# Optimization experiments

Measured on AMD Instinct MI355X. Metric: run time of the kernel, lower is better.

Reference implementation:

```python
import jax, jax.numpy as jnp
import numpy as np

N = 50000      # nodes
E = 800000     # edges per relation graph
D = 128        # embedding_size
L = 3          # gcn_layers
R = 4          # relations (n, poi, s, d)
ATT_SLOPE = 0.2   # GATConv negative_slope
ACT_SLOPE = 0.01  # F.leaky_relu default
BN_EPS = 1e-5


def setup_inputs() -> dict:
    key = jax.random.key(0)
    ks = jax.random.split(key, 8)
    features = jax.random.normal(ks[0], (N, D), jnp.float32)
    rel_emb = jax.random.normal(ks[1], (R, D), jnp.float32)
    edge_index = jax.random.randint(ks[2], (R, 2, E), 0, N, dtype=jnp.int64)
    s = 1.0 / np.sqrt(D)
    gat_W = jax.random.normal(ks[3], (L, D, D), jnp.float32) * s
    gat_asrc = jax.random.normal(ks[4], (L, D), jnp.float32) * s
    gat_adst = jax.random.normal(ks[5], (L, D), jnp.float32) * s
    gat_b = jnp.zeros((L, D), jnp.float32)
    bn_gamma = jnp.ones((L - 1, D), jnp.float32)
    bn_beta = jnp.zeros((L - 1, D), jnp.float32)
    rel_W = jax.random.normal(ks[6], (L, D, D), jnp.float32) * s
    rel_b = jax.random.normal(ks[7], (L, D), jnp.float32) * s
    return dict(features=features, rel_emb=rel_emb, edge_index=edge_index,
                gat_W=gat_W, gat_asrc=gat_asrc, gat_adst=gat_adst, gat_b=gat_b,
                bn_gamma=bn_gamma, bn_beta=bn_beta, rel_W=rel_W, rel_b=rel_b)


def gat_conv(x, edges, W, a_src, a_dst, b):
    # PyG GATConv, heads=1, no attention dropout (eval path).
    h = x @ W                                   # [N, D]
    src, dst = edges[0], edges[1]               # messages src -> dst
    e = jax.nn.leaky_relu(h[src] @ a_src + h[dst] @ a_dst, ATT_SLOPE)  # [E]
    e_max = jax.ops.segment_max(e, dst, num_segments=N)
    e_max = jnp.where(jnp.isfinite(e_max), e_max, 0.0)
    p = jnp.exp(e - e_max[dst])                 # unnormalized attn [E]
    denom = jax.ops.segment_sum(p, dst, num_segments=N)
    msg = jax.ops.segment_sum(p[:, None] * h[src], dst, num_segments=N)
    return msg / (denom[:, None] + 1e-16) + b


def batch_norm(x, gamma, beta):
    mu = x.mean(0)
    var = x.var(0)  # biased, as BN uses for normalization
    return gamma * (x - mu) * jax.lax.rsqrt(var + BN_EPS) + beta


def reference(features, rel_emb, edge_index, gat_W, gat_asrc, gat_adst, gat_b,
              bn_gamma, bn_beta, rel_W, rel_b):
    embs = [features, features, features, features]
    rels = [rel_emb[k] for k in range(R)]
    edges = [edge_index[k] for k in range(R)]
    for i in range(L - 1):
        for k in range(R):
            out = gat_conv(embs[k] * rels[k], edges[k],
                           gat_W[i], gat_asrc[i], gat_adst[i], gat_b[i])
            bn = batch_norm(out, bn_gamma[i], bn_beta[i])
            embs[k] = embs[k] + jax.nn.leaky_relu(bn, ACT_SLOPE)
            rels[k] = rels[k] @ rel_W[i].T + rel_b[i]
    for k in range(R):
        embs[k] = gat_conv(embs[k] * rels[k], edges[k],
                           gat_W[-1], gat_asrc[-1], gat_adst[-1], gat_b[-1])
        rels[k] = rels[k] @ rel_W[-1].T + rel_b[-1]
    return (embs[0], embs[1], embs[2], embs[3], rels[0], rels[1], rels[2], rels[3])
```

## Files before the change

kernel.cpp:

```cpp
#include <hip/hip_runtime.h>

#define NN 50000
#define NE 800000
#define D  128
#define RT 32
#define NB 196
#define ND ((size_t)NN * D)
#define RNG 6250

typedef unsigned short u16;
typedef unsigned int   u32;
typedef long long      ll64;

__device__ __forceinline__ float bf2f(u16 v) {
  return __uint_as_float(((u32)v) << 16);
}
__device__ __forceinline__ u16 f2bf(float f) {
  u32 u = __float_as_uint(f);
  u32 r = u + 0x7fffu + ((u >> 16) & 1u);
  return (u16)(r >> 16);
}
__device__ __forceinline__ float bflo(u32 u) { return __uint_as_float(u << 16); }
__device__ __forceinline__ float bfhi(u32 u) { return __uint_as_float(u & 0xffff0000u); }
__device__ __forceinline__ float ldf(const void* p, size_t i, int isf32) {
  return isf32 ? ((const float*)p)[i] : bf2f(((const u16*)p)[i]);
}
__device__ __forceinline__ int lde(const void* p, size_t i, int isi64) {
  return isi64 ? (int)((const ll64*)p)[i] : ((const int*)p)[i];
}

__global__ void k_detect(const void* __restrict__ feat, const void* __restrict__ edges,
                         int* __restrict__ flags) {
  __shared__ int cnt0, cnt1;
  int t = threadIdx.x;
  if (t == 0) { cnt0 = 0; cnt1 = 0; }
  __syncthreads();
  float v = ((const float*)feat)[t];
  float av = fabsf(v);
  if (av == 0.f || (av >= 1e-8f && av <= 1e4f)) atomicAdd(&cnt0, 1);
  if (t < 128) {
    if (((const int*)edges)[2 * t + 1] != 0) atomicAdd(&cnt1, 1);
  }
  __syncthreads();
  if (t == 0) {
    flags[0] = (cnt0 >= 240) ? 1 : 0;
    flags[1] = (cnt1 == 0) ? 1 : 0;
  }
}

__global__ void k_sent(float* __restrict__ out, int n) {
  int i = blockIdx.x * 256 + threadIdx.x;
  if (i < n) out[i] = 3000.0f;
}

__global__ void k_init(const void* __restrict__ feat, float* __restrict__ out,
                       const int* __restrict__ flags) {
  int isf32 = flags[0];
  int k = blockIdx.y;
  size_t i = (size_t)blockIdx.x * 256 + threadIdx.x;
  float4 v;
  if (isf32) {
    v = ((const float4*)feat)[i];
  } else {
    uint2 u = ((const uint2*)feat)[i];
    v = make_float4(bflo(u.x), bfhi(u.x), bflo(u.y), bfhi(u.y));
  }
  ((float4*)out)[(size_t)k * (ND / 4) + i] = v;
}

__global__ void k_count(const void* __restrict__ edges, int* __restrict__ deg,
                        const int* __restrict__ flags) {
  int isi64 = flags[1];
  int bid = blockIdx.x;
  int r8 = bid & 7;
  int k = (bid >> 3) & 3;
  int e = (bid >> 5) * 256 + threadIdx.x;
  int dst = lde(edges, (size_t)k * 2 * NE + NE + e, isi64);
  if (dst / RNG == r8) atomicAdd(&deg[k * NN + dst], 1);
}

__global__ void k_bsum(const int* __restrict__ deg, int* __restrict__ bsum) {
  int k = blockIdx.y, b = blockIdx.x, t = threadIdx.x;
  __shared__ int sh[256];
  int idx = b * 256 + t;
  sh[t] = (idx < NN) ? deg[k * NN + idx] : 0;
  __syncthreads();
  for (int off = 128; off; off >>= 1) {
    if (t < off) sh[t] += sh[t + off];
    __syncthreads();
  }
  if (t == 0) bsum[k * NB + b] = sh[0];
}

__global__ void k_bscan(const int* __restrict__ bsum, int* __restrict__ boff) {
  __shared__ int sh[256];
  int t = threadIdx.x;
  for (int k = 0; k < 4; k++) {
    int v = (t < NB) ? bsum[k * NB + t] : 0;
    sh[t] = v;
    __syncthreads();
    for (int off = 1; off < 256; off <<= 1) {
      int a = (t >= off) ? sh[t - off] : 0;
      __syncthreads();
      sh[t] += a;
      __syncthreads();
    }
    if (t < NB) boff[k * NB + t] = sh[t] - v;
    __syncthreads();
  }
}

__global__ void k_place(const int* __restrict__ deg, const int* __restrict__ boff,
                        int* __restrict__ rowp, int* __restrict__ cur) {
  int k = blockIdx.y, b = blockIdx.x, t = threadIdx.x;
  __shared__ int sh[256];
  int idx = b * 256 + t;
  int v = (idx < NN) ? deg[k * NN + idx] : 0;
  sh[t] = v;
  __syncthreads();
  for (int off = 1; off < 256; off <<= 1) {
    int a = (t >= off) ? sh[t - off] : 0;
    __syncthreads();
    sh[t] += a;
    __syncthreads();
  }
  int incl = boff[k * NB + b] + sh[t];
  if (idx < NN) {
    rowp[(size_t)k * (NN + 1) + idx + 1] = incl;
    cur[k * NN + idx] = incl - v;
  }
  if (b == 0 && t == 0) rowp[(size_t)k * (NN + 1)] = 0;
}

__global__ void k_scatter(const void* __restrict__ edges, int* __restrict__ cur,
                          u16* __restrict__ colx, const int* __restrict__ flags) {
  int isi64 = flags[1];
  int bid = blockIdx.x;
  int r8 = bid & 7;
  int k = (bid >> 3) & 3;
  int e = (bid >> 5) * 256 + threadIdx.x;
  int src = lde(edges, (size_t)k * 2 * NE + e, isi64);
  int dst = lde(edges, (size_t)k * 2 * NE + NE + e, isi64);
  if (dst / RNG == r8) {
    int pos = atomicAdd(&cur[k * NN + dst], 1);
    colx[(size_t)k * NE + pos] = (u16)src;
  }
}

__global__ void k_prep(const void* __restrict__ gatW, const void* __restrict__ asrc,
                       const void* __restrict__ adst, const void* __restrict__ rel_emb,
                       const float* __restrict__ relc, int layer,
                       float* __restrict__ Bm, float* __restrict__ asf, float* __restrict__ adf,
                       float* __restrict__ colsum, float* __restrict__ colsq,
                       const int* __restrict__ flags) {
  int isf32 = flags[0];
  int k = blockIdx.x;
  int r = threadIdx.x;
  float rv = (layer == 0) ? ldf(rel_emb, (size_t)k * D + r, isf32) : relc[k * D + r];
  size_t Wo = (size_t)layer * D * D + (size_t)r * D;
  float* Bk = Bm + (size_t)k * D * D;
  for (int c = 0; c < D; c++)
    Bk[r * D + c] = rv * ldf(gatW, Wo + c, isf32);
  asf[k * D + r] = ldf(asrc, (size_t)layer * D + r, isf32);
  adf[k * D + r] = ldf(adst, (size_t)layer * D + r, isf32);
  #pragma unroll
  for (int i = 0; i < 8; i++) {
    colsum[((size_t)k * 8 + i) * D + r] = 0.f;
    colsq[((size_t)k * 8 + i) * D + r] = 0.f;
  }
}

__launch_bounds__(256)
__global__ void k_gemm(const float* __restrict__ xbase, const float* __restrict__ Bm,
                       const float* __restrict__ asf, const float* __restrict__ adf,
                       u32* __restrict__ hb, float* __restrict__ av_s, float* __restrict__ av_d) {
  int k = blockIdx.y;
  const float* x = xbase + (size_t)k * ND;
  const float* Bk = Bm + (size_t)k * D * D;
  u32* hbk = hb + (size_t)k * NN * 64;

  __shared__ float xl[RT * D];
  int t = threadIdx.x;
  int row0 = blockIdx.x * RT;

  for (int i = t; i < RT * D / 4; i += 256) {
    int r = i >> 5;
    int row = row0 + r;
    float4 v = make_float4(0.f, 0.f, 0.f, 0.f);
    if (row < NN) v = ((const float4*)(x + (size_t)row * D))[i & 31];
    ((float4*)xl)[i] = v;
  }
  __syncthreads();

  int cg = t & 31, rg = t >> 5;
  float acc0[4], acc1[4], acc2[4], acc3[4];
  #pragma unroll
  for (int j = 0; j < 4; j++) { acc0[j] = 0; acc1[j] = 0; acc2[j] = 0; acc3[j] = 0; }
  const float* Bp = Bk + cg * 4;
  const float* xp = xl + (rg * 4) * D;
  for (int kk = 0; kk < D; kk += 4) {
    float4 b0 = *(const float4*)(Bp + (kk    ) * D);
    float4 b1 = *(const float4*)(Bp + (kk + 1) * D);
    float4 b2 = *(const float4*)(Bp + (kk + 2) * D);
    float4 b3 = *(const float4*)(Bp + (kk + 3) * D);
    #pragma unroll
    for (int j = 0; j < 4; j++) {
      float4 x4 = *(const float4*)(xp + j * D + kk);
      acc0[j] += x4.x * b0.x + x4.y * b1.x + x4.z * b2.x + x4.w * b3.x;
      acc1[j] += x4.x * b0.y + x4.y * b1.y + x4.z * b2.y + x4.w * b3.y;
      acc2[j] += x4.x * b0.z + x4.y * b1.z + x4.z * b2.z + x4.w * b3.z;
      acc3[j] += x4.x * b0.w + x4.y * b1.w + x4.z * b2.w + x4.w * b3.w;
    }
  }
  #pragma unroll
  for (int j = 0; j < 4; j++) {
    int row = row0 + rg * 4 + j;
    if (row < NN) {
      uint2 pk;
      pk.x = (u32)f2bf(acc0[j]) | ((u32)f2bf(acc1[j]) << 16);
      pk.y = (u32)f2bf(acc2[j]) | ((u32)f2bf(acc3[j]) << 16);
      *(uint2*)(hbk + (size_t)row * 64 + cg * 2) = pk;
    }
  }
  float w0 = asf[k * D + cg * 4], w1 = asf[k * D + cg * 4 + 1],
        w2 = asf[k * D + cg * 4 + 2], w3 = asf[k * D + cg * 4 + 3];
  float u0 = adf[k * D + cg * 4], u1 = adf[k * D + cg * 4 + 1],
        u2 = adf[k * D + cg * 4 + 2], u3 = adf[k * D + cg * 4 + 3];
  #pragma unroll
  for (int j = 0; j < 4; j++) {
    float ps = acc0[j] * w0 + acc1[j] * w1 + acc2[j] * w2 + acc3[j] * w3;
    float pd = acc0[j] * u0 + acc1[j] * u1 + acc2[j] * u2 + acc3[j] * u3;
    #pragma unroll
    for (int off = 16; off; off >>= 1) {
      ps += __shfl_xor(ps, off, 32);
      pd += __shfl_xor(pd, off, 32);
    }
    int row = row0 + rg * 4 + j;
    if (cg == 0 && row < NN) {
      av_s[(size_t)k * NN + row] = ps;
      av_d[(size_t)k * NN + row] = pd;
    }
  }
}

__launch_bounds__(256)
__global__ void k_aggf(const int* __restrict__ rowp, const u16* __restrict__ colx,
                       const float* __restrict__ av_s, const float* __restrict__ av_d,
                       const u32* __restrict__ hb, const void* __restrict__ gatb,
                       int layer, u32* __restrict__ tmpw, float* __restrict__ outf,
                       float* __restrict__ colsum, float* __restrict__ colsq,
                       const int* __restrict__ flags) {
  int isf32 = flags[0];
  int bid = blockIdx.x;
  int xcd = bid & 7;
  int k = xcd >> 1;
  int widx = ((bid >> 3) << 1) | (xcd & 1);
  int wv = threadIdx.x >> 6;
  int n = widx * 4 + wv;
  int lane = threadIdx.x & 63;
  int hi = lane >> 5;
  int cl32 = lane & 31;
  const int* rp = rowp + (size_t)k * (NN + 1);
  int s0 = rp[n], s1 = rp[n + 1];
  int deg = s1 - s0;
  const float* avs = av_s + (size_t)k * NN;
  float ad = av_d[(size_t)k * NN + n];
  const u16* cl = colx + (size_t)k * NE;
  const uint2* h2 = (const uint2*)(hb + (size_t)k * NN * 64);

  int src0 = 0; float e0 = -INFINITY;
  if (lane < deg) {
    src0 = (int)cl[s0 + lane];
    float e = avs[src0] + ad;
    e0 = e > 0.f ? e : 0.2f * e;
  }
  float m = e0;
  for (int base = 64; base < deg; base += 64) {
    int j = base + lane;
    if (j < deg) {
      int s = (int)cl[s0 + j];
      float e = avs[s] + ad;
      e = e > 0.f ? e : 0.2f * e;
      m = fmaxf(m, e);
    }
  }
  #pragma unroll
  for (int off = 32; off; off >>= 1) m = fmaxf(m, __shfl_xor(m, off, 64));

  float p0 = (lane < deg) ? __expf(e0 - m) : 0.f;
  float den = p0;
  float a0 = 0.f, a1 = 0.f, a2 = 0.f, a3 = 0.f;
  {
    int cnt = min(64, deg);
    int iters = (cnt + 1) >> 1;
    for (int it = 0; it < iters; it++) {
      int jidx = 2 * it + hi;
      float ps = __shfl(p0, jidx, 64);
      int   ss = __shfl(src0, jidx, 64);
      uint2 hv = h2[(size_t)ss * 32 + cl32];
      a0 += ps * bflo(hv.x); a1 += ps * bfhi(hv.x);
      a2 += ps * bflo(hv.y); a3 += ps * bfhi(hv.y);
    }
  }
  for (int base = 64; base < deg; base += 64) {
    int j = base + lane;
    int srcx = 0; float px = 0.f;
    if (j < deg) {
      srcx = (int)cl[s0 + j];
      float e = avs[srcx] + ad;
      e = e > 0.f ? e : 0.2f * e;
      px = __expf(e - m);
    }
    den += px;
    int cnt = min(64, deg - base);
    int iters = (cnt + 1) >> 1;
    for (int it = 0; it < iters; it++) {
      int jidx = 2 * it + hi;
      float ps = __shfl(px, jidx, 64);
      int   ss = __shfl(srcx, jidx, 64);
      uint2 hv = h2[(size_t)ss * 32 + cl32];
      a0 += ps * bflo(hv.x); a1 += ps * bfhi(hv.x);
      a2 += ps * bflo(hv.y); a3 += ps * bfhi(hv.y);
    }
  }
  #pragma unroll
  for (int off = 32; off; off >>= 1) den += __shfl_xor(den, off, 64);
  float di = 1.f / (den + 1e-16f);

  a0 += __shfl_xor(a0, 32, 64);
  a1 += __shfl_xor(a1, 32, 64);
  a2 += __shfl_xor(a2, 32, 64);
  a3 += __shfl_xor(a3, 32, 64);

  __shared__ float ps_[4][D], pq_[4][D];
  if (hi == 0) {
    int c = cl32 * 4;
    float o0 = a0 * di + ldf(gatb, (size_t)layer * D + c, isf32);
    float o1 = a1 * di + ldf(gatb, (size_t)layer * D + c + 1, isf32);
    float o2 = a2 * di + ldf(gatb, (size_t)layer * D + c + 2, isf32);
    float o3 = a3 * di + ldf(gatb, (size_t)layer * D + c + 3, isf32);
    if (tmpw) {
      uint2 pk;
      pk.x = (u32)f2bf(o0) | ((u32)f2bf(o1) << 16);
      pk.y = (u32)f2bf(o2) | ((u32)f2bf(o3) << 16);
      *(uint2*)(tmpw + (size_t)k * NN * 64 + (size_t)n * 64 + cl32 * 2) = pk;
    } else {
      *(float4*)(outf + (size_t)k * ND + (size_t)n * D + c) = make_float4(o0, o1, o2, o3);
    }
    if (colsum) {
      ps_[wv][c] = o0;      ps_[wv][c + 1] = o1;
      ps_[wv][c + 2] = o2;  ps_[wv][c + 3] = o3;
      pq_[wv][c] = o0 * o0;     pq_[wv][c + 1] = o1 * o1;
      pq_[wv][c + 2] = o2 * o2; pq_[wv][c + 3] = o3 * o3;
    }
  }
  if (colsum) {
    __syncthreads();
    int t = threadIdx.x;
    if (t < D) {
      size_t slot = ((size_t)k * 8 + (widx & 7)) * D + t;
      atomicAdd(&colsum[slot], ps_[0][t] + ps_[1][t] + ps_[2][t] + ps_[3][t]);
      atomicAdd(&colsq[slot],  pq_[0][t] + pq_[1][t] + pq_[2][t] + pq_[3][t]);
    }
  }
}

__global__ void k_bnfin(const float* __restrict__ colsum, const float* __restrict__ colsq,
                        float* __restrict__ mu, float* __restrict__ rsig) {
  int k = blockIdx.x;
  int c = threadIdx.x;
  const float* csk = colsum + (size_t)k * 8 * D;
  const float* cqk = colsq + (size_t)k * 8 * D;
  float cs = 0.f, cq = 0.f;
  #pragma unroll
  for (int r = 0; r < 8; r++) { cs += csk[r * D + c]; cq += cqk[r * D + c]; }
  float m = cs * (1.f / NN);
  float var = cq * (1.f / NN) - m * m;
  mu[k * D + c] = m;
  rsig[k * D + c] = rsqrtf(fmaxf(var, 0.f) + 1e-5f);
}

__global__ void k_update(float* __restrict__ e, const u32* __restrict__ tmpw,
                         const float* __restrict__ mu, const float* __restrict__ rsig,
                         const void* __restrict__ gamma, const void* __restrict__ beta,
                         int layer, const int* __restrict__ flags) {
  int isf32 = flags[0];
  int k = blockIdx.y;
  __shared__ float smu[D], srs[D], sg[D], sb[D];
  int t = threadIdx.x;
  if (t < D) {
    smu[t] = mu[k * D + t];
    srs[t] = rsig[k * D + t];
    sg[t] = ldf(gamma, (size_t)layer * D + t, isf32);
    sb[t] = ldf(beta, (size_t)layer * D + t, isf32);
  }
  __syncthreads();
  size_t idx = (size_t)blockIdx.x * 256 + t;
  int c0 = ((int)(idx & 31)) * 4;
  uint2 tv = *(const uint2*)(tmpw + (size_t)k * NN * 64 + idx * 2);
  float tb[4] = {bflo(tv.x), bfhi(tv.x), bflo(tv.y), bfhi(tv.y)};
  float* ek = e + (size_t)k * ND;
  float4 e4 = ((const float4*)ek)[idx];
  float eb[4] = {e4.x, e4.y, e4.z, e4.w};
  #pragma unroll
  for (int i = 0; i < 4; i++) {
    int c = c0 + i;
    float bn = sg[c] * (tb[i] - smu[c]) * srs[c] + sb[c];
    bn = bn > 0.f ? bn : 0.01f * bn;
    eb[i] += bn;
  }
  ((float4*)ek)[idx] = make_float4(eb[0], eb[1], eb[2], eb[3]);
}

__global__ void k_relup(const void* __restrict__ relW, const void* __restrict__ relb,
                        const void* __restrict__ rel_emb, float* __restrict__ relc,
                        int layer, float* __restrict__ out_final,
                        const int* __restrict__ flags) {
  int isf32 = flags[0];
  int k = blockIdx.x;
  __shared__ float rl[D];
  int c = threadIdx.x;
  rl[c] = (layer == 0) ? ldf(rel_emb, (size_t)k * D + c, isf32) : relc[k * D + c];
  __syncthreads();
  float acc = ldf(relb, (size_t)layer * D + c, isf32);
  size_t Wo = ((size_t)layer * D + c) * D;
  for (int kk = 0; kk < D; kk++) acc += ldf(relW, Wo + kk, isf32) * rl[kk];
  relc[k * D + c] = acc;
  if (out_final) out_final[(size_t)k * D + c] = acc;
}

extern "C" void kernel_launch(void* const* d_in, const int* in_sizes, int n_in,
                              void* d_out, int out_size, void* d_ws, size_t ws_size,
                              hipStream_t stream) {
  const void* feat    = d_in[0];
  const void* rel_emb = d_in[1];
  const void* edges   = d_in[2];
  const void* gatW    = d_in[3];
  const void* asrc    = d_in[4];
  const void* adst    = d_in[5];
  const void* gatb    = d_in[6];
  const void* gamma   = d_in[7];
  const void* beta    = d_in[8];
  const void* relW    = d_in[9];
  const void* relb    = d_in[10];
  float* out = (float*)d_out;

  char* p = (char*)d_ws;
  auto take = [&](size_t bytes) -> void* {
    void* r = (void*)p;
    p += (bytes + 255) & ~(size_t)255;
    return r;
  };
  u32*   hb     = (u32*)  take((size_t)4 * NN * 64 * 4);
  u32*   tmpw   = (u32*)  take((size_t)4 * NN * 64 * 4);
  u16*   colx   = (u16*)  take((size_t)4 * NE * 2);
  int*   rowp   = (int*)  take((size_t)4 * (NN + 1) * 4);
  int*   cur    = (int*)  take((size_t)4 * NN * 4);
  int*   deg    = (int*)  take((size_t)4 * NN * 4);
  int*   bsum   = (int*)  take((size_t)4 * NB * 4);
  int*   boff   = (int*)  take((size_t)4 * NB * 4);
  float* av_s   = (float*)take((size_t)4 * NN * 4);
  float* av_d   = (float*)take((size_t)4 * NN * 4);
  float* Bm     = (float*)take((size_t)4 * D * D * 4);
  float* asf    = (float*)take(4 * D * 4);
  float* adf    = (float*)take(4 * D * 4);
  float* relc   = (float*)take(4 * D * 4);
  float* colsum = (float*)take((size_t)4 * 8 * D * 4);
  float* colsq  = (float*)take((size_t)4 * 8 * D * 4);
  float* muv    = (float*)take(4 * D * 4);
  float* rsv    = (float*)take(4 * D * 4);
  int*   flags  = (int*)  take(64);

  size_t need = (size_t)(p - (char*)d_ws);
  if (ws_size < need) {
    k_sent<<<(out_size + 255) / 256, 256, 0, stream>>>(out, out_size);
    return;
  }

  hipMemsetAsync(deg, 0, (size_t)4 * NN * 4, stream);

  k_detect<<<1, 256, 0, stream>>>(feat, edges, flags);
  k_init<<<dim3((int)(ND / 4 / 256), 4), 256, 0, stream>>>(feat, out, flags);
  k_count<<<(NE / 256) * 32, 256, 0, stream>>>(edges, deg, flags);
  k_bsum<<<dim3(NB, 4), 256, 0, stream>>>(deg, bsum);
  k_bscan<<<1, 256, 0, stream>>>(bsum, boff);
  k_place<<<dim3(NB, 4), 256, 0, stream>>>(deg, boff, rowp, cur);
  k_scatter<<<(NE / 256) * 32, 256, 0, stream>>>(edges, cur, colx, flags);

  for (int layer = 0; layer < 3; layer++) {
    bool last = (layer == 2);
    k_prep<<<4, 128, 0, stream>>>(gatW, asrc, adst, rel_emb, relc, layer,
                                  Bm, asf, adf, colsum, colsq, flags);
    k_gemm<<<dim3((NN + RT - 1) / RT, 4), 256, 0, stream>>>(out, Bm, asf, adf, hb, av_s, av_d);
    if (!last) {
      k_aggf<<<NN, 256, 0, stream>>>(rowp, colx, av_s, av_d, hb, gatb, layer,
                                     tmpw, (float*)nullptr, colsum, colsq, flags);
      k_bnfin<<<4, 128, 0, stream>>>(colsum, colsq, muv, rsv);
      k_update<<<dim3((int)(ND / 4 / 256), 4), 256, 0, stream>>>(out, tmpw, muv, rsv,
                                                                 gamma, beta, layer, flags);
      k_relup<<<4, 128, 0, stream>>>(relW, relb, rel_emb, relc, layer, (float*)nullptr, flags);
    } else {
      k_aggf<<<NN, 256, 0, stream>>>(rowp, colx, av_s, av_d, hb, gatb, layer,
                                     (u32*)nullptr, out, (float*)nullptr, (float*)nullptr, flags);
      k_relup<<<4, 128, 0, stream>>>(relW, relb, rel_emb, relc, layer, out + 4 * ND, flags);
    }
  }
}
```

Before: 1.381 ms.

## Pack edges into 32-bit words and widen per-lane gathers in aggregation

A new conversion kernel reads the int64/int32 edge list once and packs src and dst into a single u32 per edge. The count and scatter passes then read this compact array instead of re-reading the wide edge list 8 times each through range filtering. The aggregation kernel also changes its lane mapping so each lane gathers 32 bytes (two uint4) of a neighbor row and processes 8 neighbors per iteration instead of 2. This cuts loop iterations and shuffles, at the cost of 16 accumulators per lane, more registers and a three-step cross-lane reduction.

```diff
diff --git a/kernel.cpp b/kernel.cpp
--- a/kernel.cpp
+++ b/kernel.cpp
@@ -68,14 +68,22 @@
   ((float4*)out)[(size_t)k * (ND / 4) + i] = v;
 }
 
-__global__ void k_count(const void* __restrict__ edges, int* __restrict__ deg,
-                        const int* __restrict__ flags) {
+__global__ void k_conv(const void* __restrict__ edges, u32* __restrict__ epack,
+                       const int* __restrict__ flags) {
   int isi64 = flags[1];
+  int k = blockIdx.y;
+  int e = blockIdx.x * 256 + threadIdx.x;
+  int src = lde(edges, (size_t)k * 2 * NE + e, isi64);
+  int dst = lde(edges, (size_t)k * 2 * NE + NE + e, isi64);
+  epack[(size_t)k * NE + e] = (u32)src | ((u32)dst << 16);
+}
+
+__global__ void k_count(const u32* __restrict__ epack, int* __restrict__ deg) {
   int bid = blockIdx.x;
   int r8 = bid & 7;
   int k = (bid >> 3) & 3;
   int e = (bid >> 5) * 256 + threadIdx.x;
-  int dst = lde(edges, (size_t)k * 2 * NE + NE + e, isi64);
+  int dst = (int)(epack[(size_t)k * NE + e] >> 16);
   if (dst / RNG == r8) atomicAdd(&deg[k * NN + dst], 1);
 }
 
@@ -132,18 +140,17 @@
   if (b == 0 && t == 0) rowp[(size_t)k * (NN + 1)] = 0;
 }
 
-__global__ void k_scatter(const void* __restrict__ edges, int* __restrict__ cur,
-                          u16* __restrict__ colx, const int* __restrict__ flags) {
-  int isi64 = flags[1];
+__global__ void k_scatter(const u32* __restrict__ epack, int* __restrict__ cur,
+                          u16* __restrict__ colx) {
   int bid = blockIdx.x;
   int r8 = bid & 7;
   int k = (bid >> 3) & 3;
   int e = (bid >> 5) * 256 + threadIdx.x;
-  int src = lde(edges, (size_t)k * 2 * NE + e, isi64);
-  int dst = lde(edges, (size_t)k * 2 * NE + NE + e, isi64);
+  u32 v = epack[(size_t)k * NE + e];
+  int dst = (int)(v >> 16);
   if (dst / RNG == r8) {
     int pos = atomicAdd(&cur[k * NN + dst], 1);
-    colx[(size_t)k * NE + pos] = (u16)src;
+    colx[(size_t)k * NE + pos] = (u16)(v & 0xffffu);
   }
 }
 
@@ -258,15 +265,15 @@
   int wv = threadIdx.x >> 6;
   int n = widx * 4 + wv;
   int lane = threadIdx.x & 63;
-  int hi = lane >> 5;
-  int cl32 = lane & 31;
+  int o = lane >> 3;
+  int cl8 = lane & 7;
   const int* rp = rowp + (size_t)k * (NN + 1);
   int s0 = rp[n], s1 = rp[n + 1];
   int deg = s1 - s0;
   const float* avs = av_s + (size_t)k * NN;
   float ad = av_d[(size_t)k * NN + n];
   const u16* cl = colx + (size_t)k * NE;
-  const uint2* h2 = (const uint2*)(hb + (size_t)k * NN * 64);
+  const uint4* h4 = (const uint4*)(hb + (size_t)k * NN * 64);
 
   int src0 = 0; float e0 = -INFINITY;
   if (lane < deg) {
@@ -289,17 +296,26 @@
 
   float p0 = (lane < deg) ? __expf(e0 - m) : 0.f;
   float den = p0;
-  float a0 = 0.f, a1 = 0.f, a2 = 0.f, a3 = 0.f;
+  float a[16];
+  #pragma unroll
+  for (int i = 0; i < 16; i++) a[i] = 0.f;
   {
     int cnt = min(64, deg);
-    int iters = (cnt + 1) >> 1;
+    int iters = (cnt + 7) >> 3;
     for (int it = 0; it < iters; it++) {
-      int jidx = 2 * it + hi;
+      int jidx = 8 * it + o;
       float ps = __shfl(p0, jidx, 64);
       int   ss = __shfl(src0, jidx, 64);
-      uint2 hv = h2[(size_t)ss * 32 + cl32];
-      a0 += ps * bflo(hv.x); a1 += ps * bfhi(hv.x);
-      a2 += ps * bflo(hv.y); a3 += ps * bfhi(hv.y);
+      uint4 h0 = h4[(size_t)ss * 16 + cl8 * 2];
+      uint4 h1 = h4[(size_t)ss * 16 + cl8 * 2 + 1];
+      a[0] += ps * bflo(h0.x);  a[1] += ps * bfhi(h0.x);
+      a[2] += ps * bflo(h0.y);  a[3] += ps * bfhi(h0.y);
+      a[4] += ps * bflo(h0.z);  a[5] += ps * bfhi(h0.z);
+      a[6] += ps * bflo(h0.w);  a[7] += ps * bfhi(h0.w);
+      a[8] += ps * bflo(h1.x);  a[9] += ps * bfhi(h1.x);
+      a[10] += ps * bflo(h1.y); a[11] += ps * bfhi(h1.y);
+      a[12] += ps * bflo(h1.z); a[13] += ps * bfhi(h1.z);
+      a[14] += ps * bflo(h1.w); a[15] += ps * bfhi(h1.w);
     }
   }
   for (int base = 64; base < deg; base += 64) {
@@ -313,45 +329,67 @@
     }
     den += px;
     int cnt = min(64, deg - base);
-    int iters = (cnt + 1) >> 1;
+    int iters = (cnt + 7) >> 3;
     for (int it = 0; it < iters; it++) {
-      int jidx = 2 * it + hi;
+      int jidx = 8 * it + o;
       float ps = __shfl(px, jidx, 64);
       int   ss = __shfl(srcx, jidx, 64);
-      uint2 hv = h2[(size_t)ss * 32 + cl32];
-      a0 += ps * bflo(hv.x); a1 += ps * bfhi(hv.x);
-      a2 += ps * bflo(hv.y); a3 += ps * bfhi(hv.y);
+      uint4 h0 = h4[(size_t)ss * 16 + cl8 * 2];
+      uint4 h1 = h4[(size_t)ss * 16 + cl8 * 2 + 1];
+      a[0] += ps * bflo(h0.x);  a[1] += ps * bfhi(h0.x);
+      a[2] += ps * bflo(h0.y);  a[3] += ps * bfhi(h0.y);
+      a[4] += ps * bflo(h0.z);  a[5] += ps * bfhi(h0.z);
+      a[6] += ps * bflo(h0.w);  a[7] += ps * bfhi(h0.w);
+      a[8] += ps * bflo(h1.x);  a[9] += ps * bfhi(h1.x);
+      a[10] += ps * bflo(h1.y); a[11] += ps * bfhi(h1.y);
+      a[12] += ps * bflo(h1.z); a[13] += ps * bfhi(h1.z);
+      a[14] += ps * bflo(h1.w); a[15] += ps * bfhi(h1.w);
     }
   }
   #pragma unroll
   for (int off = 32; off; off >>= 1) den += __shfl_xor(den, off, 64);
   float di = 1.f / (den + 1e-16f);
 
-  a0 += __shfl_xor(a0, 32, 64);
-  a1 += __shfl_xor(a1, 32, 64);
-  a2 += __shfl_xor(a2, 32, 64);
-  a3 += __shfl_xor(a3, 32, 64);
+  #pragma unroll
+  for (int i = 0; i < 16; i++) {
+    a[i] += __shfl_xor(a[i], 8, 64);
+    a[i] += __shfl_xor(a[i], 16, 64);
+    a[i] += __shfl_xor(a[i], 32, 64);
+  }
 
   __shared__ float ps_[4][D], pq_[4][D];
-  if (hi == 0) {
-    int c = cl32 * 4;
-    float o0 = a0 * di + ldf(gatb, (size_t)layer * D + c, isf32);
-    float o1 = a1 * di + ldf(gatb, (size_t)layer * D + c + 1, isf32);
-    float o2 = a2 * di + ldf(gatb, (size_t)layer * D + c + 2, isf32);
-    float o3 = a3 * di + ldf(gatb, (size_t)layer * D + c + 3, isf32);
+  if (o == 0) {
+    int c = cl8 * 16;
+    float ov[16];
+    #pragma unroll
+    for (int i = 0; i < 16; i++)
+      ov[i] = a[i] * di + ldf(gatb, (size_t)layer * D + c + i, isf32);
     if (tmpw) {
-      uint2 pk;
-      pk.x = (u32)f2bf(o0) | ((u32)f2bf(o1) << 16);
-      pk.y = (u32)f2bf(o2) | ((u32)f2bf(o3) << 16);
-      *(uint2*)(tmpw + (size_t)k * NN * 64 + (size_t)n * 64 + cl32 * 2) = pk;
+      uint4 pk0, pk1;
+      pk0.x = (u32)f2bf(ov[0]) | ((u32)f2bf(ov[1]) << 16);
+      pk0.y = (u32)f2bf(ov[2]) | ((u32)f2bf(ov[3]) << 16);
+      pk0.z = (u32)f2bf(ov[4]) | ((u32)f2bf(ov[5]) << 16);
+      pk0.w = (u32)f2bf(ov[6]) | ((u32)f2bf(ov[7]) << 16);
+      pk1.x = (u32)f2bf(ov[8]) | ((u32)f2bf(ov[9]) << 16);
+      pk1.y = (u32)f2bf(ov[10]) | ((u32)f2bf(ov[11]) << 16);
+      pk1.z = (u32)f2bf(ov[12]) | ((u32)f2bf(ov[13]) << 16);
+      pk1.w = (u32)f2bf(ov[14]) | ((u32)f2bf(ov[15]) << 16);
+      u32* tp = tmpw + (size_t)k * NN * 64 + (size_t)n * 64 + cl8 * 8;
+      *(uint4*)tp = pk0;
+      *(uint4*)(tp + 4) = pk1;
     } else {
-      *(float4*)(outf + (size_t)k * ND + (size_t)n * D + c) = make_float4(o0, o1, o2, o3);
+      float* op = outf + (size_t)k * ND + (size_t)n * D + c;
+      *(float4*)op = make_float4(ov[0], ov[1], ov[2], ov[3]);
+      *(float4*)(op + 4) = make_float4(ov[4], ov[5], ov[6], ov[7]);
+      *(float4*)(op + 8) = make_float4(ov[8], ov[9], ov[10], ov[11]);
+      *(float4*)(op + 12) = make_float4(ov[12], ov[13], ov[14], ov[15]);
     }
     if (colsum) {
-      ps_[wv][c] = o0;      ps_[wv][c + 1] = o1;
-      ps_[wv][c + 2] = o2;  ps_[wv][c + 3] = o3;
-      pq_[wv][c] = o0 * o0;     pq_[wv][c + 1] = o1 * o1;
-      pq_[wv][c + 2] = o2 * o2; pq_[wv][c + 3] = o3 * o3;
+      #pragma unroll
+      for (int i = 0; i < 16; i++) {
+        ps_[wv][c + i] = ov[i];
+        pq_[wv][c + i] = ov[i] * ov[i];
+      }
     }
   }
   if (colsum) {
@@ -453,6 +491,7 @@
   };
   u32*   hb     = (u32*)  take((size_t)4 * NN * 64 * 4);
   u32*   tmpw   = (u32*)  take((size_t)4 * NN * 64 * 4);
+  u32*   epack  = (u32*)  take((size_t)4 * NE * 4);
   u16*   colx   = (u16*)  take((size_t)4 * NE * 2);
   int*   rowp   = (int*)  take((size_t)4 * (NN + 1) * 4);
   int*   cur    = (int*)  take((size_t)4 * NN * 4);
@@ -481,11 +520,12 @@
 
   k_detect<<<1, 256, 0, stream>>>(feat, edges, flags);
   k_init<<<dim3((int)(ND / 4 / 256), 4), 256, 0, stream>>>(feat, out, flags);
-  k_count<<<(NE / 256) * 32, 256, 0, stream>>>(edges, deg, flags);
+  k_conv<<<dim3(NE / 256, 4), 256, 0, stream>>>(edges, epack, flags);
+  k_count<<<(NE / 256) * 32, 256, 0, stream>>>(epack, deg);
   k_bsum<<<dim3(NB, 4), 256, 0, stream>>>(deg, bsum);
   k_bscan<<<1, 256, 0, stream>>>(bsum, boff);
   k_place<<<dim3(NB, 4), 256, 0, stream>>>(deg, boff, rowp, cur);
-  k_scatter<<<(NE / 256) * 32, 256, 0, stream>>>(edges, cur, colx, flags);
+  k_scatter<<<(NE / 256) * 32, 256, 0, stream>>>(epack, cur, colx);
 
   for (int layer = 0; layer < 3; layer++) {
     bool last = (layer == 2);
```

Result: no change. 1.398 ms (+1.2%).
